# Kernel tuning notes

Measured on AMD Instinct MI355X. Metric: run time of the kernel, lower is better.

## Reference

```python
import jax, jax.numpy as jnp
import numpy as np

B, S, HID = 1, 2048, 4096
NH, NKV, HD = 32, 8, 128
WINDOW = 1024
ROPE_THETA = 1e6
NEG = -1e9


def rotate_half(x):
    x1, x2 = jnp.split(x, 2, axis=-1)
    return jnp.concatenate((-x2, x1), axis=-1)


def setup_inputs() -> dict:
    key = jax.random.key(0)
    ks = jax.random.split(key, 10)
    hidden_states = jax.random.normal(ks[0], (B, S, HID), jnp.float32)
    # rotary tables [max_pos, head_dim]
    inv_freq = 1.0 / (ROPE_THETA ** (jnp.arange(0, HD, 2, dtype=jnp.float32) / HD))
    t = jnp.arange(S, dtype=jnp.float32)
    freqs = jnp.outer(t, inv_freq)                       # [S, HD/2]
    emb = jnp.concatenate((freqs, freqs), axis=-1)       # [S, HD]
    cos, sin = jnp.cos(emb), jnp.sin(emb)
    position_ids = jnp.arange(S, dtype=jnp.int64)[None, :].astype(jnp.int32)
    # sliding-window causal additive mask [B,1,S,S]
    i = jnp.arange(S)[:, None]
    j = jnp.arange(S)[None, :]
    allowed = (j <= i) & (j > i - WINDOW)
    attention_mask = jnp.where(allowed, 0.0, NEG).astype(jnp.float32)[None, None]
    sc = 0.02
    Wq = jax.random.normal(ks[1], (HID, NH * HD), jnp.float32) * sc
    bq = jax.random.normal(ks[2], (NH * HD,), jnp.float32) * sc
    Wk = jax.random.normal(ks[3], (HID, NKV * HD), jnp.float32) * sc
    bk = jax.random.normal(ks[4], (NKV * HD,), jnp.float32) * sc
    Wv = jax.random.normal(ks[5], (HID, NKV * HD), jnp.float32) * sc
    bv = jax.random.normal(ks[6], (NKV * HD,), jnp.float32) * sc
    Wo = jax.random.normal(ks[7], (NH * HD, HID), jnp.float32) * sc
    bo = jax.random.normal(ks[8], (HID,), jnp.float32) * sc
    return dict(hidden_states=hidden_states, attention_mask=attention_mask,
                position_ids=position_ids, cos=cos, sin=sin,
                Wq=Wq, bq=bq, Wk=Wk, bk=bk, Wv=Wv, bv=bv, Wo=Wo, bo=bo)


def reference(hidden_states, attention_mask, position_ids, cos, sin,
              Wq, bq, Wk, bk, Wv, bv, Wo, bo):
    bsz, q_len, _ = hidden_states.shape
    q = (hidden_states @ Wq + bq).reshape(bsz, q_len, NH, HD).transpose(0, 2, 1, 3)
    k = (hidden_states @ Wk + bk).reshape(bsz, q_len, NKV, HD).transpose(0, 2, 1, 3)
    v = (hidden_states @ Wv + bv).reshape(bsz, q_len, NKV, HD).transpose(0, 2, 1, 3)
    # RoPE: cos/sin gathered by position_ids -> [B,1,S,HD]
    c = cos[position_ids][:, None]
    s = sin[position_ids][:, None]
    q = q * c + rotate_half(q) * s
    k = k * c + rotate_half(k) * s
    # GQA repeat_kv: [B,NKV,S,HD] -> [B,NH,S,HD]
    n_rep = NH // NKV
    k = jnp.repeat(k, n_rep, axis=1)
    v = jnp.repeat(v, n_rep, axis=1)
    scores = jnp.einsum('bhqd,bhkd->bhqk', q, k) / np.sqrt(HD).astype(np.float32)
    scores = scores + attention_mask[:, :, :, :k.shape[2]]
    probs = jax.nn.softmax(scores.astype(jnp.float32), axis=-1).astype(q.dtype)
    attn = jnp.einsum('bhqk,bhkd->bhqd', probs, v)
    attn = attn.transpose(0, 2, 1, 3).reshape(bsz, q_len, NH * HD)
    return attn @ Wo + bo
```

## Files before the change

### kernel.cpp

```cpp
#include <hip/hip_runtime.h>
#include <stdint.h>

typedef unsigned short u16;
typedef __attribute__((ext_vector_type(4))) float f32x4;
typedef __attribute__((ext_vector_type(16))) float f32x16;
typedef __attribute__((ext_vector_type(8))) __bf16 bf16x8;
typedef __attribute__((ext_vector_type(4))) u16 u16x4;
typedef __attribute__((ext_vector_type(8))) u16 u16x8;
typedef __attribute__((ext_vector_type(4))) unsigned int u32x4;

#define S_LEN 2048
#define HIDDEN 4096
#define NHEAD 32
#define NKVH 8
#define HD 128
#define WIN 1024

__device__ __forceinline__ float bf2f(u16 u) {
  union { unsigned int i; float f; } x; x.i = ((unsigned int)u) << 16; return x.f;
}
__device__ __forceinline__ u16 f2bf(float f) {
  union { float f; unsigned int i; } x; x.f = f;
  unsigned int r = x.i + 0x7FFFu + ((x.i >> 16) & 1u);
  return (u16)(r >> 16);
}

__device__ __forceinline__ void gload16(const void* g, void* l) {
  __builtin_amdgcn_global_load_lds((const __attribute__((address_space(1))) void*)g,
                                   (__attribute__((address_space(3))) void*)l, 16, 0, 0);
}

__device__ __forceinline__ unsigned int cvtpk_bf16(float a, float b) {
  unsigned int w;
  asm("v_cvt_pk_bf16_f32 %0, %1, %2" : "=v"(w) : "v"(a), "v"(b));
  return w;
}

__device__ __forceinline__ void transp_f32(const float* __restrict__ in, int istride,
                                           u16* __restrict__ out, int ostride,
                                           int bx, int by, char* smem) {
  float (*tile)[68] = (float (*)[68])smem;
  int r0 = bx * 64, c0 = by * 64;
  int t = threadIdx.x;
  int tr = t >> 4;
  int tc = (t & 15) * 4;
#pragma unroll
  for (int i = 0; i < 4; ++i) {
    int r = i * 16 + tr;
    *(f32x4*)&tile[r][tc] = *(const f32x4*)(in + (size_t)(r0 + r) * istride + c0 + tc);
  }
  __syncthreads();
#pragma unroll
  for (int i = 0; i < 4; ++i) {
    int rr = i * 16 + tr;
    u16x4 o;
#pragma unroll
    for (int j = 0; j < 4; ++j) o[j] = f2bf(tile[tc + j][rr]);
    *(u16x4*)(out + (size_t)(c0 + rr) * ostride + r0 + tc) = o;
  }
}

__global__ __launch_bounds__(256) void prep_k(const float* __restrict__ X,
                                              const float* __restrict__ Wq, const float* __restrict__ Wk,
                                              const float* __restrict__ Wv,
                                              const float* __restrict__ bq, const float* __restrict__ bk,
                                              const float* __restrict__ bv,
                                              u16* __restrict__ Xb, u16* __restrict__ WT,
                                              float* __restrict__ bqkv) {
  __shared__ __align__(16) char smem[17408];
  int bid = blockIdx.x;
  if (bid < 4096) {
    size_t i = ((size_t)bid * 256 + threadIdx.x) * 8;
    f32x4 a = *(const f32x4*)(X + i);
    f32x4 b = *(const f32x4*)(X + i + 4);
    u16x8 o;
    o[0] = f2bf(a[0]); o[1] = f2bf(a[1]); o[2] = f2bf(a[2]); o[3] = f2bf(a[3]);
    o[4] = f2bf(b[0]); o[5] = f2bf(b[1]); o[6] = f2bf(b[2]); o[7] = f2bf(b[3]);
    *(u16x8*)(Xb + i) = o;
  } else if (bid < 8192) {
    int tt = bid - 4096;
    transp_f32(Wq, 4096, WT, 4096, tt & 63, tt >> 6, smem);
  } else if (bid < 9216) {
    int tt = bid - 8192;
    transp_f32(Wk, 1024, WT + (size_t)4096 * 4096, 4096, tt & 63, tt >> 6, smem);
  } else if (bid < 10240) {
    int tt = bid - 9216;
    transp_f32(Wv, 1024, WT + (size_t)5120 * 4096, 4096, tt & 63, tt >> 6, smem);
  } else {
    int i = (bid - 10240) * 256 + threadIdx.x;
    float v = (i < 4096) ? bq[i] : (i < 5120 ? bk[i - 4096] : bv[i - 5120]);
    bqkv[i] = v;
  }
}

__global__ __launch_bounds__(256, 3) void gemmqkv_k(const u16* __restrict__ A, const u16* __restrict__ Bt,
                                                    const float* __restrict__ bias,
                                                    const int* __restrict__ pos,
                                                    const float* __restrict__ cosT, const float* __restrict__ sinT,
                                                    u16* __restrict__ Q, u16* __restrict__ Kf,
                                                    u16* __restrict__ Vf, int K) {
  constexpr int NL = 4;
  __shared__ __align__(16) u16 SM[24576];
  u16* SA = SM;
  u16* SB = SM + 12288;

  int tid = threadIdx.x;
  int w = tid >> 6, l = tid & 63;
  int cl = l & 15, g = l >> 4;
  int wr = w >> 1, wc = w & 1;

  int cpx = gridDim.x >> 3;
  int wg = (blockIdx.x & 7) * cpx + (blockIdx.x >> 3);
  int bm = wg & 15, bn = wg >> 4;

  const u16* Ag = A + (size_t)(bm * 128) * K;
  const u16* Bg = Bt + (size_t)(bn * 128) * K;
  int srow = w * 16 + (l >> 2);
  int csrc = ((l & 3) ^ ((l >> 3) & 3)) * 8;
  int rdc = (g ^ ((cl >> 1) & 3)) << 3;

  f32x4 acc[4][4] = {};
  int NT = K >> 5;

  auto stage = [&](int slot, int tt, int h) {
    if (h < 2) {
      gload16(Ag + (size_t)(h * 64 + srow) * K + tt * 32 + csrc,
              (void*)(SA + slot * 4096 + (h * 64 + w * 16) * 32));
    } else {
      int hb = h - 2;
      gload16(Bg + (size_t)(hb * 64 + srow) * K + tt * 32 + csrc,
              (void*)(SB + slot * 4096 + (hb * 64 + w * 16) * 32));
    }
  };

#pragma unroll
  for (int h = 0; h < NL; ++h) stage(0, 0, h);
#pragma unroll
  for (int h = 0; h < NL; ++h) stage(1, 1, h);

  for (int t = 0; t < NT; ++t) {
    asm volatile("s_waitcnt vmcnt(4)" ::: "memory");
    __builtin_amdgcn_s_barrier();
    asm volatile("" ::: "memory");

    int slot = t % 3, ss = (t + 2) % 3;
    int ts = t + 2; if (ts >= NT) ts -= NT;
#pragma unroll
    for (int h = 0; h < NL; ++h) stage(ss, ts, h);

    const u16* sa = SA + slot * 4096;
    const u16* sb = SB + slot * 4096;
    bf16x8 af[4], bf[4];
#pragma unroll
    for (int mi = 0; mi < 4; ++mi)
      af[mi] = *(const bf16x8*)(sa + (wr * 64 + mi * 16 + cl) * 32 + rdc);
#pragma unroll
    for (int ni = 0; ni < 4; ++ni)
      bf[ni] = *(const bf16x8*)(sb + (wc * 64 + ni * 16 + cl) * 32 + rdc);
    __builtin_amdgcn_s_setprio(1);
#pragma unroll
    for (int mi = 0; mi < 4; ++mi)
#pragma unroll
      for (int ni = 0; ni < 4; ++ni)
        acc[mi][ni] = __builtin_amdgcn_mfma_f32_16x16x32_bf16(af[mi], bf[ni], acc[mi][ni], 0, 0, 0);
    __builtin_amdgcn_s_setprio(0);
  }

  asm volatile("s_waitcnt vmcnt(0)" ::: "memory");
  __syncthreads();

  u16 (*tileL)[132] = (u16 (*)[132])SM;
#pragma unroll
  for (int mi = 0; mi < 4; ++mi)
#pragma unroll
    for (int ni = 0; ni < 4; ++ni) {
      int col = wc * 64 + ni * 16 + cl;
      float bb = bias[bn * 128 + col];
#pragma unroll
      for (int r = 0; r < 4; ++r)
        tileL[wr * 64 + mi * 16 + g * 4 + r][col] = f2bf(acc[mi][ni][r] + bb);
    }
  __syncthreads();

  int s0 = bm * 128;
  if (bn < 32) {
    int hq = bn;
    int r = tid >> 1, u = tid & 1;
    int s = s0 + r;
    int ps = pos[s];
    const float* cb = cosT + (size_t)ps * 128;
    const float* sb = sinT + (size_t)ps * 128;
    u16* dst = Q + ((size_t)hq * S_LEN + s) * HD;
    const float qs = 0.08838834764831845f;
#pragma unroll
    for (int c8 = 0; c8 < 4; ++c8) {
      int d0 = u * 32 + c8 * 8;
      u16x8 lo, hi;
#pragma unroll
      for (int j = 0; j < 8; ++j) {
        int d = d0 + j;
        float x0 = bf2f(tileL[r][d]);
        float x1 = bf2f(tileL[r][d + 64]);
        lo[j] = f2bf((x0 * cb[d] - x1 * sb[d]) * qs);
        hi[j] = f2bf((x1 * cb[d + 64] + x0 * sb[d + 64]) * qs);
      }
      *(u16x8*)(dst + d0) = lo;
      *(u16x8*)(dst + d0 + 64) = hi;
    }
  } else if (bn < 40) {
    int kh = bn - 32;
    int r = tid >> 1, u = tid & 1;
    int s = s0 + r;
    int ps = pos[s];
    const float* cb = cosT + (size_t)ps * 128;
    const float* sb = sinT + (size_t)ps * 128;
    int t2 = s >> 5, cr = s & 31;
#pragma unroll
    for (int c8 = 0; c8 < 4; ++c8) {
      int d0 = u * 32 + c8 * 8;
      u16x8 lo, hi;
#pragma unroll
      for (int j = 0; j < 8; ++j) {
        int d = d0 + j;
        float x0 = bf2f(tileL[r][d]);
        float x1 = bf2f(tileL[r][d + 64]);
        lo[j] = f2bf(x0 * cb[d] - x1 * sb[d]);
        hi[j] = f2bf(x1 * cb[d + 64] + x0 * sb[d + 64]);
      }
      size_t base_lo = ((size_t)(kh * 64 + t2) * 8 + (d0 >> 4)) * 512 + (size_t)(cr + 32 * ((d0 >> 3) & 1)) * 8;
      *(u16x8*)(Kf + base_lo) = lo;
      int dh = d0 + 64;
      size_t base_hi = ((size_t)(kh * 64 + t2) * 8 + (dh >> 4)) * 512 + (size_t)(cr + 32 * ((dh >> 3) & 1)) * 8;
      *(u16x8*)(Kf + base_hi) = hi;
    }
  } else {
    int kh = bn - 40;
#pragma unroll
    for (int i = 0; i < 8; ++i) {
      int c = i * 256 + tid;
      int lv = c & 63, sl = (c >> 6) & 1, dt = (c >> 7) & 3, t2l = c >> 9;
      int h2 = lv >> 5, c2 = lv & 31;
      int rl = t2l * 32 + sl * 16 + h2 * 8;
      int colv = dt * 32 + c2;
      u16x8 o;
#pragma unroll
      for (int j = 0; j < 8; ++j) o[j] = tileL[rl + j][colv];
      size_t addr = ((size_t)(kh * 512 + (bm * 4 + t2l) * 8 + dt * 2 + sl)) * 512 + (size_t)lv * 8;
      *(u16x8*)(Vf + addr) = o;
    }
  }
}

template <int BM, int BN, int MINW, typename TOUT>
__global__ __launch_bounds__(256, MINW) void gemm4_k(const u16* __restrict__ A, const u16* __restrict__ Bt,
                                                     const float* __restrict__ bias, TOUT* __restrict__ C,
                                                     int M, int N, int K) {
  constexpr int WM = BM / 2, WN = BN / 2;
  constexpr int MRA = WM / 16, MRB = WN / 16;
  constexpr int NA = BM / 64, NB = BN / 64;
  constexpr int NL = NA + NB;
  __shared__ __align__(16) u16 SA[3 * BM * 32];
  __shared__ __align__(16) u16 SB[3 * BN * 32];

  int tid = threadIdx.x;
  int w = tid >> 6, l = tid & 63;
  int cl = l & 15, g = l >> 4;
  int wr = w >> 1, wc = w & 1;

  int cpx = gridDim.x >> 3;
  int wg = (blockIdx.x & 7) * cpx + (blockIdx.x >> 3);
  int nbm = M / BM;
  int bm = wg % nbm, bn = wg / nbm;

  const u16* Ag = A + (size_t)(bm * BM) * K;
  const u16* Bg = Bt + (size_t)(bn * BN) * K;
  int srow = w * 16 + (l >> 2);
  int csrc = ((l & 3) ^ ((l >> 3) & 3)) * 8;
  int rdc = (g ^ ((cl >> 1) & 3)) << 3;

  f32x4 acc[MRA][MRB] = {};
  int NT = K >> 5;

  auto stage = [&](int slot, int tt, int h) {
    if (h < NA) {
      gload16(Ag + (size_t)(h * 64 + srow) * K + tt * 32 + csrc,
              (void*)(SA + slot * (BM * 32) + (h * 64 + w * 16) * 32));
    } else {
      int hb = h - NA;
      gload16(Bg + (size_t)(hb * 64 + srow) * K + tt * 32 + csrc,
              (void*)(SB + slot * (BN * 32) + (hb * 64 + w * 16) * 32));
    }
  };

#pragma unroll
  for (int h = 0; h < NL; ++h) stage(0, 0, h);
#pragma unroll
  for (int h = 0; h < NL; ++h) stage(1, 1, h);

  for (int t = 0; t < NT; ++t) {
    if constexpr (NL == 5) asm volatile("s_waitcnt vmcnt(5)" ::: "memory");
    else if constexpr (NL == 4) asm volatile("s_waitcnt vmcnt(4)" ::: "memory");
    else asm volatile("s_waitcnt vmcnt(3)" ::: "memory");
    __builtin_amdgcn_s_barrier();
    asm volatile("" ::: "memory");

    int slot = t % 3, ss = (t + 2) % 3;
    int ts = t + 2; if (ts >= NT) ts -= NT;
#pragma unroll
    for (int h = 0; h < NL; ++h) stage(ss, ts, h);

    const u16* sa = SA + slot * (BM * 32);
    const u16* sb = SB + slot * (BN * 32);
    bf16x8 af[MRA], bf[MRB];
#pragma unroll
    for (int mi = 0; mi < MRA; ++mi)
      af[mi] = *(const bf16x8*)(sa + (wr * WM + mi * 16 + cl) * 32 + rdc);
#pragma unroll
    for (int ni = 0; ni < MRB; ++ni)
      bf[ni] = *(const bf16x8*)(sb + (wc * WN + ni * 16 + cl) * 32 + rdc);
    __builtin_amdgcn_s_setprio(1);
#pragma unroll
    for (int mi = 0; mi < MRA; ++mi)
#pragma unroll
      for (int ni = 0; ni < MRB; ++ni)
        acc[mi][ni] = __builtin_amdgcn_mfma_f32_16x16x32_bf16(af[mi], bf[ni], acc[mi][ni], 0, 0, 0);
    __builtin_amdgcn_s_setprio(0);
  }

  asm volatile("s_waitcnt vmcnt(0)" ::: "memory");

#pragma unroll
  for (int mi = 0; mi < MRA; ++mi) {
    int row0 = bm * BM + wr * WM + mi * 16 + g * 4;
#pragma unroll
    for (int ni = 0; ni < MRB; ++ni) {
      int col = bn * BN + wc * WN + ni * 16 + cl;
      float bb = bias[col];
      f32x4 a = acc[mi][ni];
#pragma unroll
      for (int r = 0; r < 4; ++r) {
        float v = a[r] + bb;
        if constexpr (sizeof(TOUT) == 2) C[(size_t)(row0 + r) * N + col] = f2bf(v);
        else C[(size_t)(row0 + r) * N + col] = v;
      }
    }
  }
}

__global__ __launch_bounds__(256, 2) void attnwot_k(const u16* __restrict__ Q, const u16* __restrict__ Kf,
                                                    const u16* __restrict__ Vf, u16* __restrict__ O,
                                                    const float* __restrict__ Wo, u16* __restrict__ WT) {
  __shared__ __align__(16) char smem[17408];
  if (blockIdx.x >= 512) {
    int tt = blockIdx.x - 512;
    transp_f32(Wo, 4096, WT, 4096, tt & 63, tt >> 6, smem);
    return;
  }
  int l = threadIdx.x & 63, w = threadIdx.x >> 6;
  int col = l & 31, hi = l >> 5;
  int bid = blockIdx.x;
  int kh = bid & 7;
  int head = (bid >> 3) & 3;
  int qbp = bid >> 5;
  int qb = (qbp & 1) ? (15 - (qbp >> 1)) : (qbp >> 1);
  int h = kh * 4 + head;
  int q0 = qb * 128 + w * 32;

  bf16x8 qf[8];
  const u16* qbase = Q + ((size_t)h * S_LEN + q0 + col) * HD + hi * 8;
#pragma unroll
  for (int ks = 0; ks < 8; ++ks) qf[ks] = *(const bf16x8*)(qbase + ks * 16);

  f32x16 ot[4];
#pragma unroll
  for (int dt = 0; dt < 4; ++dt)
#pragma unroll
    for (int r = 0; r < 16; ++r) ot[dt][r] = 0.f;
  float m_r = -3.0e38f, l_r = 0.f;

  const u16* kf0 = Kf + (size_t)kh * 64 * 4096 + (size_t)l * 8;
  const u16* vf0 = Vf + (size_t)kh * 512 * 512 + (size_t)l * 8;

  int jstart = q0 >= WIN ? q0 - WIN : 0;
  bf16x8 kfr[8];
  {
    const u16* kb = kf0 + (size_t)(jstart >> 5) * 4096;
#pragma unroll
    for (int ks = 0; ks < 8; ++ks) kfr[ks] = *(const bf16x8*)(kb + ks * 512);
  }

  for (int j0 = jstart; j0 <= q0; j0 += 32) {
    int t = j0 >> 5;
    f32x16 sA = {}, sB = {};
#pragma unroll
    for (int ks = 0; ks < 4; ++ks)
      sA = __builtin_amdgcn_mfma_f32_32x32x16_bf16(kfr[ks], qf[ks], sA, 0, 0, 0);
#pragma unroll
    for (int ks = 4; ks < 8; ++ks)
      sB = __builtin_amdgcn_mfma_f32_32x32x16_bf16(kfr[ks], qf[ks], sB, 0, 0, 0);
    int tn = (j0 + 32 <= q0) ? (t + 1) : t;
    const u16* kbn = kf0 + (size_t)tn * 4096;
    bf16x8 kfn[8];
#pragma unroll
    for (int ks = 0; ks < 8; ++ks) kfn[ks] = *(const bf16x8*)(kbn + ks * 512);
    const u16* vb = vf0 + (size_t)t * 4096;
    bf16x8 vfr[8];
#pragma unroll
    for (int c = 0; c < 8; ++c) vfr[c] = *(const bf16x8*)(vb + c * 512);

    f32x16 s = sA + sB;

    if (j0 + 31 > q0 || j0 < q0 - 992) {
      int q = q0 + col;
#pragma unroll
      for (int r = 0; r < 16; ++r) {
        int kv = j0 + (r & 3) + 8 * (r >> 2) + 4 * hi;
        if (kv > q || kv <= q - WIN) s[r] = -3.0e38f;
      }
    }
    float vm = fmaxf(fmaxf(fmaxf(s[0], s[1]), fmaxf(s[2], s[3])),
                     fmaxf(fmaxf(s[4], s[5]), fmaxf(s[6], s[7])));
    vm = fmaxf(vm, fmaxf(fmaxf(fmaxf(s[8], s[9]), fmaxf(s[10], s[11])),
                         fmaxf(fmaxf(s[12], s[13]), fmaxf(s[14], s[15]))));
    vm = fmaxf(vm, __shfl_xor(vm, 32));
    float mnew = fmaxf(m_r, vm);
    float sc = __expf(m_r - mnew);
    m_r = mnew;
    float rs = 0.f;
#pragma unroll
    for (int r = 0; r < 16; ++r) {
      float pv = __expf(s[r] - mnew);
      s[r] = pv;
      rs += pv;
    }
    rs += __shfl_xor(rs, 32);
    l_r = l_r * sc + rs;
#pragma unroll
    for (int dt = 0; dt < 4; ++dt)
#pragma unroll
      for (int r = 0; r < 16; ++r) ot[dt][r] *= sc;

    bf16x8 pb[2];
#pragma unroll
    for (int sl = 0; sl < 2; ++sl) {
      int b = sl * 8;
      unsigned int a0 = cvtpk_bf16(s[b + 0], s[b + 1]);
      unsigned int c0 = cvtpk_bf16(s[b + 4], s[b + 5]);
      asm("v_permlane32_swap_b32 %0, %1" : "+v"(a0), "+v"(c0));
      unsigned int a1 = cvtpk_bf16(s[b + 2], s[b + 3]);
      unsigned int c1 = cvtpk_bf16(s[b + 6], s[b + 7]);
      asm("v_permlane32_swap_b32 %0, %1" : "+v"(a1), "+v"(c1));
      u32x4 pv = {a0, a1, c0, c1};
      pb[sl] = __builtin_bit_cast(bf16x8, pv);
    }
#pragma unroll
    for (int dt = 0; dt < 4; ++dt) {
      ot[dt] = __builtin_amdgcn_mfma_f32_32x32x16_bf16(vfr[dt * 2 + 0], pb[0], ot[dt], 0, 0, 0);
      ot[dt] = __builtin_amdgcn_mfma_f32_32x32x16_bf16(vfr[dt * 2 + 1], pb[1], ot[dt], 0, 0, 0);
    }
#pragma unroll
    for (int ks = 0; ks < 8; ++ks) kfr[ks] = kfn[ks];
  }

  float inv = 1.0f / l_r;
#pragma unroll
  for (int dt = 0; dt < 4; ++dt) {
#pragma unroll
    for (int g2 = 0; g2 < 4; ++g2) {
      u16x4 o;
#pragma unroll
      for (int i = 0; i < 4; ++i) o[i] = f2bf(ot[dt][g2 * 4 + i] * inv);
      *(u16x4*)(O + (size_t)(q0 + col) * HIDDEN + h * HD + dt * 32 + g2 * 8 + hi * 4) = o;
    }
  }
}

extern "C" void kernel_launch(void* const* d_in, const int* in_sizes, int n_in,
                              void* d_out, int out_size, void* d_ws, size_t ws_size,
                              hipStream_t stream) {
  const float* X = (const float*)d_in[0];
  const int* pos = (const int*)d_in[2];
  const float* cosT = (const float*)d_in[3];
  const float* sinT = (const float*)d_in[4];
  const float* Wq = (const float*)d_in[5];
  const float* bq = (const float*)d_in[6];
  const float* Wk = (const float*)d_in[7];
  const float* bk = (const float*)d_in[8];
  const float* Wv = (const float*)d_in[9];
  const float* bv = (const float*)d_in[10];
  const float* Wo = (const float*)d_in[11];
  const float* bo = (const float*)d_in[12];
  float* out = (float*)d_out;

  const size_t MB = 1ull << 20;
  char* ws = (char*)d_ws;
  u16* WT = (u16*)ws;
  u16* Xb = (u16*)(ws + 48 * MB);
  u16* attnO = Xb;
  u16* Qs = (u16*)(ws + 64 * MB);
  u16* Kfr = (u16*)(ws + 88 * MB);
  u16* Vfr = (u16*)(ws + 92 * MB);
  float* bqkv = (float*)(ws + 96 * MB);

  prep_k<<<10264, 256, 0, stream>>>(X, Wq, Wk, Wv, bq, bk, bv, Xb, WT, bqkv);

  gemmqkv_k<<<768, 256, 0, stream>>>(Xb, WT, bqkv, pos, cosT, sinT, Qs, Kfr, Vfr, 4096);

  attnwot_k<<<4608, 256, 0, stream>>>(Qs, Kfr, Vfr, attnO, Wo, WT);

  gemm4_k<128, 128, 3, float><<<512, 256, 0, stream>>>(attnO, WT, bo, out, 2048, 4096, 4096);
}
```

Measured before the change: 321.1 us.

## Enlarge fused QKV GEMM tile to 256x256 with 512-thread blocks

The QKV projection GEMM now uses 256x256 output tiles with 8 waves per block instead of 128x128 with 4 waves. Each wave computes 128x64, and the launch drops from 768 to 192 blocks. The epilogue (bias, RoPE, Q scaling, K/V fragment layout) runs in two 128-row halves through a reused LDS tile, with vectorized LDS reads. The larger tile is meant to raise operand reuse and cut global/LDS traffic per FLOP. In exchange, 192 blocks give less than one wave of work on a 256-CU device, and each block needs more registers and LDS.

```diff
diff --git a/kernel.cpp b/kernel.cpp
--- a/kernel.cpp
+++ b/kernel.cpp
@@ -93,50 +93,49 @@
   }
 }
 
-__global__ __launch_bounds__(256, 3) void gemmqkv_k(const u16* __restrict__ A, const u16* __restrict__ Bt,
+__global__ __launch_bounds__(512, 2) void gemmqkv_k(const u16* __restrict__ A, const u16* __restrict__ Bt,
                                                     const float* __restrict__ bias,
                                                     const int* __restrict__ pos,
                                                     const float* __restrict__ cosT, const float* __restrict__ sinT,
                                                     u16* __restrict__ Q, u16* __restrict__ Kf,
                                                     u16* __restrict__ Vf, int K) {
-  constexpr int NL = 4;
-  __shared__ __align__(16) u16 SM[24576];
+  __shared__ __align__(16) u16 SM[49152];
   u16* SA = SM;
-  u16* SB = SM + 12288;
+  u16* SB = SM + 24576;
 
   int tid = threadIdx.x;
   int w = tid >> 6, l = tid & 63;
   int cl = l & 15, g = l >> 4;
-  int wr = w >> 1, wc = w & 1;
+  int wr = w >> 2, wc = w & 3;
 
   int cpx = gridDim.x >> 3;
   int wg = (blockIdx.x & 7) * cpx + (blockIdx.x >> 3);
-  int bm = wg & 15, bn = wg >> 4;
-
-  const u16* Ag = A + (size_t)(bm * 128) * K;
-  const u16* Bg = Bt + (size_t)(bn * 128) * K;
+  int bm = wg & 7, bn = wg >> 3;
+
+  const u16* Ag = A + (size_t)(bm * 256) * K;
+  const u16* Bg = Bt + (size_t)(bn * 256) * K;
   int srow = w * 16 + (l >> 2);
   int csrc = ((l & 3) ^ ((l >> 3) & 3)) * 8;
   int rdc = (g ^ ((cl >> 1) & 3)) << 3;
 
-  f32x4 acc[4][4] = {};
+  f32x4 acc[8][4] = {};
   int NT = K >> 5;
 
-  auto stage = [&](int slot, int tt, int h) {
-    if (h < 2) {
-      gload16(Ag + (size_t)(h * 64 + srow) * K + tt * 32 + csrc,
-              (void*)(SA + slot * 4096 + (h * 64 + w * 16) * 32));
+  auto stage = [&](int slot, int tt, int u) {
+    if (u < 2) {
+      gload16(Ag + (size_t)(u * 128 + srow) * K + tt * 32 + csrc,
+              (void*)(SA + slot * 8192 + u * 4096 + w * 512));
     } else {
-      int hb = h - 2;
-      gload16(Bg + (size_t)(hb * 64 + srow) * K + tt * 32 + csrc,
-              (void*)(SB + slot * 4096 + (hb * 64 + w * 16) * 32));
+      int ub = u - 2;
+      gload16(Bg + (size_t)(ub * 128 + srow) * K + tt * 32 + csrc,
+              (void*)(SB + slot * 8192 + ub * 4096 + w * 512));
     }
   };
 
 #pragma unroll
-  for (int h = 0; h < NL; ++h) stage(0, 0, h);
-#pragma unroll
-  for (int h = 0; h < NL; ++h) stage(1, 1, h);
+  for (int u = 0; u < 4; ++u) stage(0, 0, u);
+#pragma unroll
+  for (int u = 0; u < 4; ++u) stage(1, 1, u);
 
   for (int t = 0; t < NT; ++t) {
     asm volatile("s_waitcnt vmcnt(4)" ::: "memory");
@@ -146,20 +145,20 @@
     int slot = t % 3, ss = (t + 2) % 3;
     int ts = t + 2; if (ts >= NT) ts -= NT;
 #pragma unroll
-    for (int h = 0; h < NL; ++h) stage(ss, ts, h);
-
-    const u16* sa = SA + slot * 4096;
-    const u16* sb = SB + slot * 4096;
-    bf16x8 af[4], bf[4];
-#pragma unroll
-    for (int mi = 0; mi < 4; ++mi)
-      af[mi] = *(const bf16x8*)(sa + (wr * 64 + mi * 16 + cl) * 32 + rdc);
+    for (int u = 0; u < 4; ++u) stage(ss, ts, u);
+
+    const u16* sa = SA + slot * 8192;
+    const u16* sb = SB + slot * 8192;
+    bf16x8 af[8], bf[4];
+#pragma unroll
+    for (int mi = 0; mi < 8; ++mi)
+      af[mi] = *(const bf16x8*)(sa + (wr * 128 + mi * 16 + cl) * 32 + rdc);
 #pragma unroll
     for (int ni = 0; ni < 4; ++ni)
       bf[ni] = *(const bf16x8*)(sb + (wc * 64 + ni * 16 + cl) * 32 + rdc);
     __builtin_amdgcn_s_setprio(1);
 #pragma unroll
-    for (int mi = 0; mi < 4; ++mi)
+    for (int mi = 0; mi < 8; ++mi)
 #pragma unroll
       for (int ni = 0; ni < 4; ++ni)
         acc[mi][ni] = __builtin_amdgcn_mfma_f32_16x16x32_bf16(af[mi], bf[ni], acc[mi][ni], 0, 0, 0);
@@ -169,85 +168,98 @@
   asm volatile("s_waitcnt vmcnt(0)" ::: "memory");
   __syncthreads();
 
-  u16 (*tileL)[132] = (u16 (*)[132])SM;
-#pragma unroll
-  for (int mi = 0; mi < 4; ++mi)
-#pragma unroll
-    for (int ni = 0; ni < 4; ++ni) {
-      int col = wc * 64 + ni * 16 + cl;
-      float bb = bias[bn * 128 + col];
-#pragma unroll
-      for (int r = 0; r < 4; ++r)
-        tileL[wr * 64 + mi * 16 + g * 4 + r][col] = f2bf(acc[mi][ni][r] + bb);
-    }
-  __syncthreads();
-
-  int s0 = bm * 128;
-  if (bn < 32) {
-    int hq = bn;
-    int r = tid >> 1, u = tid & 1;
-    int s = s0 + r;
-    int ps = pos[s];
-    const float* cb = cosT + (size_t)ps * 128;
-    const float* sb = sinT + (size_t)ps * 128;
-    u16* dst = Q + ((size_t)hq * S_LEN + s) * HD;
-    const float qs = 0.08838834764831845f;
-#pragma unroll
-    for (int c8 = 0; c8 < 4; ++c8) {
-      int d0 = u * 32 + c8 * 8;
-      u16x8 lo, hi;
-#pragma unroll
-      for (int j = 0; j < 8; ++j) {
-        int d = d0 + j;
-        float x0 = bf2f(tileL[r][d]);
-        float x1 = bf2f(tileL[r][d + 64]);
-        lo[j] = f2bf((x0 * cb[d] - x1 * sb[d]) * qs);
-        hi[j] = f2bf((x1 * cb[d + 64] + x0 * sb[d + 64]) * qs);
+  u16 (*tileL)[264] = (u16 (*)[264])SM;
+  const float qs = 0.08838834764831845f;
+#pragma unroll
+  for (int hp = 0; hp < 2; ++hp) {
+    if (wr == hp) {
+#pragma unroll
+      for (int mi = 0; mi < 8; ++mi)
+#pragma unroll
+        for (int ni = 0; ni < 4; ++ni) {
+          int col = wc * 64 + ni * 16 + cl;
+          float bb = bias[bn * 256 + col];
+#pragma unroll
+          for (int r = 0; r < 4; ++r)
+            tileL[mi * 16 + g * 4 + r][col] = f2bf(acc[mi][ni][r] + bb);
+        }
+    }
+    __syncthreads();
+
+    int s0 = bm * 256 + hp * 128;
+    if (bn < 16) {
+      int r = tid >> 2, u2 = tid & 3;
+      int hl = u2 >> 1, u = u2 & 1;
+      int hq = bn * 2 + hl;
+      int s = s0 + r;
+      int ps = pos[s];
+      const float* cb = cosT + (size_t)ps * 128;
+      const float* sb = sinT + (size_t)ps * 128;
+      u16* dst = Q + ((size_t)hq * S_LEN + s) * HD;
+#pragma unroll
+      for (int c8 = 0; c8 < 4; ++c8) {
+        int d0 = u * 32 + c8 * 8;
+        u16x8 xlo = *(const u16x8*)&tileL[r][hl * 128 + d0];
+        u16x8 xhi = *(const u16x8*)&tileL[r][hl * 128 + d0 + 64];
+        u16x8 lo, hi;
+#pragma unroll
+        for (int j = 0; j < 8; ++j) {
+          int d = d0 + j;
+          float x0 = bf2f(xlo[j]);
+          float x1 = bf2f(xhi[j]);
+          lo[j] = f2bf((x0 * cb[d] - x1 * sb[d]) * qs);
+          hi[j] = f2bf((x1 * cb[d + 64] + x0 * sb[d + 64]) * qs);
+        }
+        *(u16x8*)(dst + d0) = lo;
+        *(u16x8*)(dst + d0 + 64) = hi;
       }
-      *(u16x8*)(dst + d0) = lo;
-      *(u16x8*)(dst + d0 + 64) = hi;
-    }
-  } else if (bn < 40) {
-    int kh = bn - 32;
-    int r = tid >> 1, u = tid & 1;
-    int s = s0 + r;
-    int ps = pos[s];
-    const float* cb = cosT + (size_t)ps * 128;
-    const float* sb = sinT + (size_t)ps * 128;
-    int t2 = s >> 5, cr = s & 31;
-#pragma unroll
-    for (int c8 = 0; c8 < 4; ++c8) {
-      int d0 = u * 32 + c8 * 8;
-      u16x8 lo, hi;
-#pragma unroll
-      for (int j = 0; j < 8; ++j) {
-        int d = d0 + j;
-        float x0 = bf2f(tileL[r][d]);
-        float x1 = bf2f(tileL[r][d + 64]);
-        lo[j] = f2bf(x0 * cb[d] - x1 * sb[d]);
-        hi[j] = f2bf(x1 * cb[d + 64] + x0 * sb[d + 64]);
+    } else if (bn < 20) {
+      int r = tid >> 2, u2 = tid & 3;
+      int hl = u2 >> 1, u = u2 & 1;
+      int kh = (bn - 16) * 2 + hl;
+      int s = s0 + r;
+      int ps = pos[s];
+      const float* cb = cosT + (size_t)ps * 128;
+      const float* sb = sinT + (size_t)ps * 128;
+      int t2 = s >> 5, cr = s & 31;
+#pragma unroll
+      for (int c8 = 0; c8 < 4; ++c8) {
+        int d0 = u * 32 + c8 * 8;
+        u16x8 xlo = *(const u16x8*)&tileL[r][hl * 128 + d0];
+        u16x8 xhi = *(const u16x8*)&tileL[r][hl * 128 + d0 + 64];
+        u16x8 lo, hi;
+#pragma unroll
+        for (int j = 0; j < 8; ++j) {
+          int d = d0 + j;
+          float x0 = bf2f(xlo[j]);
+          float x1 = bf2f(xhi[j]);
+          lo[j] = f2bf(x0 * cb[d] - x1 * sb[d]);
+          hi[j] = f2bf(x1 * cb[d + 64] + x0 * sb[d + 64]);
+        }
+        size_t base_lo = ((size_t)(kh * 64 + t2) * 8 + (d0 >> 4)) * 512 + (size_t)(cr + 32 * ((d0 >> 3) & 1)) * 8;
+        *(u16x8*)(Kf + base_lo) = lo;
+        int dh = d0 + 64;
+        size_t base_hi = ((size_t)(kh * 64 + t2) * 8 + (dh >> 4)) * 512 + (size_t)(cr + 32 * ((dh >> 3) & 1)) * 8;
+        *(u16x8*)(Kf + base_hi) = hi;
       }
-      size_t base_lo = ((size_t)(kh * 64 + t2) * 8 + (d0 >> 4)) * 512 + (size_t)(cr + 32 * ((d0 >> 3) & 1)) * 8;
-      *(u16x8*)(Kf + base_lo) = lo;
-      int dh = d0 + 64;
-      size_t base_hi = ((size_t)(kh * 64 + t2) * 8 + (dh >> 4)) * 512 + (size_t)(cr + 32 * ((dh >> 3) & 1)) * 8;
-      *(u16x8*)(Kf + base_hi) = hi;
-    }
-  } else {
-    int kh = bn - 40;
-#pragma unroll
-    for (int i = 0; i < 8; ++i) {
-      int c = i * 256 + tid;
-      int lv = c & 63, sl = (c >> 6) & 1, dt = (c >> 7) & 3, t2l = c >> 9;
-      int h2 = lv >> 5, c2 = lv & 31;
-      int rl = t2l * 32 + sl * 16 + h2 * 8;
-      int colv = dt * 32 + c2;
-      u16x8 o;
-#pragma unroll
-      for (int j = 0; j < 8; ++j) o[j] = tileL[rl + j][colv];
-      size_t addr = ((size_t)(kh * 512 + (bm * 4 + t2l) * 8 + dt * 2 + sl)) * 512 + (size_t)lv * 8;
-      *(u16x8*)(Vf + addr) = o;
-    }
+    } else {
+#pragma unroll
+      for (int i = 0; i < 8; ++i) {
+        int c = i * 512 + tid;
+        int lv = c & 63, sl = (c >> 6) & 1, dt = (c >> 7) & 3;
+        int t_local = (c >> 9) & 3, hl = c >> 11;
+        int kh = (bn - 20) * 2 + hl;
+        int rl = t_local * 32 + sl * 16 + (lv >> 5) * 8;
+        int colv = hl * 128 + dt * 32 + (lv & 31);
+        u16x8 o;
+#pragma unroll
+        for (int j = 0; j < 8; ++j) o[j] = tileL[rl + j][colv];
+        int tglob = bm * 8 + hp * 4 + t_local;
+        size_t addr = ((size_t)(kh * 512 + tglob * 8 + dt * 2 + sl)) * 512 + (size_t)lv * 8;
+        *(u16x8*)(Vf + addr) = o;
+      }
+    }
+    __syncthreads();
   }
 }
 
@@ -504,7 +516,7 @@
 
   prep_k<<<10264, 256, 0, stream>>>(X, Wq, Wk, Wv, bq, bk, bv, Xb, WT, bqkv);
 
-  gemmqkv_k<<<768, 256, 0, stream>>>(Xb, WT, bqkv, pos, cosT, sinT, Qs, Kfr, Vfr, 4096);
+  gemmqkv_k<<<192, 512, 0, stream>>>(Xb, WT, bqkv, pos, cosT, sinT, Qs, Kfr, Vfr, 4096);
 
   attnwot_k<<<4608, 256, 0, stream>>>(Qs, Kfr, Vfr, attnO, Wo, WT);
 
```

Measured after the change: 301.1 us. 6.2% less time.
